# Performance work log

Measured on AMD Instinct MI355X. Metric: run time of the kernel, lower is better.

## Reference

```python
import itertools
import jax, jax.numpy as jnp
import numpy as np

N = 6          # particles per spin channel -> 720 permutations
D = 3          # spatial dim
HID = 64
BATCH = 2048


def _perms_and_signs(n):
    """All n! permutations in lexicographic order + their signs (+1/-1)."""
    perms = np.array(list(itertools.permutations(range(n))), dtype=np.int32)
    i, j = np.triu_indices(n, 1)
    inversions = (perms[:, i] > perms[:, j]).sum(axis=1)
    signs = np.where(inversions % 2 == 0, 1.0, -1.0).astype(np.float32)
    return jnp.asarray(perms), jnp.asarray(signs)


def setup_inputs() -> dict:
    key = jax.random.key(0)
    ks = jax.random.split(key, 6)
    scale1 = 1.0 / np.sqrt(N * D)
    scale2 = 1.0 / np.sqrt(HID)
    return {
        "x1": jax.random.normal(ks[0], (BATCH, N, D), dtype=jnp.float32),
        "x2": jax.random.normal(ks[1], (BATCH, N, D), dtype=jnp.float32),
        "W1a": jax.random.normal(ks[2], (N * D, HID), dtype=jnp.float32) * scale1,
        "b1a": jnp.zeros((HID,), dtype=jnp.float32),
        "W2a": jax.random.normal(ks[3], (HID, 1), dtype=jnp.float32) * scale2,
        "b2a": jnp.zeros((1,), dtype=jnp.float32),
        "W1b": jax.random.normal(ks[4], (N * D, HID), dtype=jnp.float32) * scale1,
        "b1b": jnp.zeros((HID,), dtype=jnp.float32),
        "W2b": jax.random.normal(ks[5], (HID, 1), dtype=jnp.float32) * scale2,
        "b2b": jnp.zeros((1,), dtype=jnp.float32),
    }


def _antisymmetrized_leaf(x, W1, b1, W2, b2):
    # x: (B, n, d). Gather all n! permutations along axis -2.
    n, d = x.shape[-2], x.shape[-1]
    perms, signs = _perms_and_signs(n)          # (n!, n), (n!,)
    x_perm = jnp.take(x, perms, axis=-2)        # (B, n!, n, d)
    x_perm = x_perm.reshape(x_perm.shape[:-2] + (n * d,))  # (B, n!, n*d)
    # fn_to_antisymmetrize: MLP (..., n*d) -> (..., 1)
    h = jnp.tanh(x_perm @ W1 + b1)              # (B, n!, HID)
    perms_out = h @ W2 + b2                     # (B, n!, 1)
    signed = signs[:, None] * perms_out         # (B, n!, 1)
    return jnp.sum(signed, axis=(-1, -2))       # (B,)


def reference(x1, x2, W1a, b1a, W2a, b2a, W1b, b1b, W2b, b2b):
    psi1 = _antisymmetrized_leaf(x1, W1a, b1a, W2a, b2a)
    psi2 = _antisymmetrized_leaf(x2, W1b, b1b, W2b, b2b)
    # logabs=True: sum_i log|psi_i|
    return jnp.log(jnp.abs(psi1)) + jnp.log(jnp.abs(psi2))
```

## Files before the change

kernel.cpp:

```cpp
#include <hip/hip_runtime.h>
#include <math.h>


typedef float  v2f __attribute__((ext_vector_type(2)));
typedef double v2d __attribute__((ext_vector_type(2)));

__device__ __forceinline__ void pin(v2f& v) { asm volatile("" : "+v"(v)); }

__device__ __forceinline__ float fexp2(float x) {
#if __has_builtin(__builtin_amdgcn_exp2f)
    return __builtin_amdgcn_exp2f(x);
#else
    return exp2f(x);
#endif
}
__device__ __forceinline__ float frcp(float x) {
#if __has_builtin(__builtin_amdgcn_rcpf)
    return __builtin_amdgcn_rcpf(x);
#else
    return 1.0f / x;
#endif
}
__device__ __forceinline__ v2f vrcp(v2f v) {
    v2f r; r.x = frcp(v.x); r.y = frcp(v.y); return r;
}
__device__ __forceinline__ v2f vfma(v2f a, v2f b, v2f c) {
    return __builtin_elementwise_fma(a, b, c);
}

constexpr int lowest_free(unsigned used) {
    for (int j = 0; j < 6; ++j)
        if (!(used & (1u << j))) return j;
    return -1;
}

#define FJI_LIST(X) X(0,0) X(0,1) X(0,2) X(0,3) X(1,0) X(1,1) X(1,2) X(1,3) \
                    X(2,0) X(2,1) X(2,2) X(2,3) X(3,0) X(3,1) X(3,2) X(3,3) \
                    X(4,0) X(4,1) X(4,2) X(4,3) X(5,0) X(5,1) X(5,2) X(5,3)
#define J6_LIST(X) X(0) X(1) X(2) X(3) X(4) X(5)
#define PAIR_LIST(X) X(0,1) X(0,2) X(0,3) X(0,4) X(0,5) X(1,2) X(1,3) X(1,4) \
                     X(1,5) X(2,3) X(2,4) X(2,5) X(3,4) X(3,5) X(4,5)
#define WC_LIST(X) X(0) X(1) X(2) X(3) X(4) X(5) X(6) X(7) X(8) X(9) X(10) \
                   X(11) X(12) X(13) X(14) X(15) X(16) X(17)

struct Tbl {
#define M(j,i) v2f F##j##_##i;
    FJI_LIST(M)
#undef M
#define M(j) v2f FA##j; v2f FB##j; v2f G##j;
    J6_LIST(M)
#undef M
#define M(a,b) v2f W##a##b; v2f S##a##b; v2f Q##a##b;
    PAIR_LIST(M)
#undef M
};

template <int J, int I> __device__ __forceinline__ v2f getF(const Tbl& T) {
#define M(j,i) if constexpr (J==j && I==i) return T.F##j##_##i;
    FJI_LIST(M)
#undef M
    __builtin_unreachable();
}
template <int J, int I> __device__ __forceinline__ void setF(Tbl& T, v2f v) {
#define M(j,i) if constexpr (J==j && I==i) T.F##j##_##i = v;
    FJI_LIST(M)
#undef M
}
template <int J> __device__ __forceinline__ v2f getFA(const Tbl& T) {
#define M(j) if constexpr (J==j) return T.FA##j;
    J6_LIST(M)
#undef M
    __builtin_unreachable();
}
template <int J> __device__ __forceinline__ void setFA(Tbl& T, v2f v) {
#define M(j) if constexpr (J==j) T.FA##j = v;
    J6_LIST(M)
#undef M
}
template <int J> __device__ __forceinline__ v2f getFB(const Tbl& T) {
#define M(j) if constexpr (J==j) return T.FB##j;
    J6_LIST(M)
#undef M
    __builtin_unreachable();
}
template <int J> __device__ __forceinline__ void setFB(Tbl& T, v2f v) {
#define M(j) if constexpr (J==j) T.FB##j = v;
    J6_LIST(M)
#undef M
}
template <int J> __device__ __forceinline__ v2f getG(const Tbl& T) {
#define M(j) if constexpr (J==j) return T.G##j;
    J6_LIST(M)
#undef M
    __builtin_unreachable();
}
template <int J> __device__ __forceinline__ void setG(Tbl& T, v2f v) {
#define M(j) if constexpr (J==j) T.G##j = v;
    J6_LIST(M)
#undef M
}
template <int A, int B> __device__ __forceinline__ v2f getW(const Tbl& T) {
#define M(a,b) if constexpr (A==a && B==b) return T.W##a##b;
    PAIR_LIST(M)
#undef M
    __builtin_unreachable();
}
template <int A, int B> __device__ __forceinline__ void setW(Tbl& T, v2f v) {
#define M(a,b) if constexpr (A==a && B==b) T.W##a##b = v;
    PAIR_LIST(M)
#undef M
}
template <int A, int B> __device__ __forceinline__ v2f getS(const Tbl& T) {
#define M(a,b) if constexpr (A==a && B==b) return T.S##a##b;
    PAIR_LIST(M)
#undef M
    __builtin_unreachable();
}
template <int A, int B> __device__ __forceinline__ void setS(Tbl& T, v2f v) {
#define M(a,b) if constexpr (A==a && B==b) T.S##a##b = v;
    PAIR_LIST(M)
#undef M
}
template <int A, int B> __device__ __forceinline__ v2f getQ(const Tbl& T) {
#define M(a,b) if constexpr (A==a && B==b) return T.Q##a##b;
    PAIR_LIST(M)
#undef M
    __builtin_unreachable();
}
template <int A, int B> __device__ __forceinline__ void setQ(Tbl& T, v2f v) {
#define M(a,b) if constexpr (A==a && B==b) T.Q##a##b = v;
    PAIR_LIST(M)
#undef M
}

struct Wgt {
#define M(r) float c##r;
    WC_LIST(M)
#undef M
    float b1s;
};
template <int R> __device__ __forceinline__ float getWC(const Wgt& W) {
#define M(r) if constexpr (R==r) return W.c##r;
    WC_LIST(M)
#undef M
    __builtin_unreachable();
}

template <int J, int I>
__device__ __forceinline__ void setupJI(Tbl& T, const Wgt& Wg,
                                        v2f x0, v2f x1, v2f x2) {
    v2f c = x0 * getWC<3*I+0>(Wg) + x1 * getWC<3*I+1>(Wg) + x2 * getWC<3*I+2>(Wg);
    if constexpr (I == 0) { c.x += Wg.b1s; c.y += Wg.b1s; }
    v2f e; e.x = fexp2(c.x); e.y = fexp2(c.y);
    if constexpr (I < 4) setF<J, I>(T, e);
    else if constexpr (I == 4) setFA<J>(T, e);
    else { setFB<J>(T, e); setG<J>(T, getFA<J>(T) * e); }
}

template <int J>
__device__ __forceinline__ void setupJ(Tbl& T, const Wgt& Wg,
                                       const float* xa, const float* xb) {
    v2f x0, x1, x2;
    x0.x = xa[3*J+0]; x0.y = xb[3*J+0];
    x1.x = xa[3*J+1]; x1.y = xb[3*J+1];
    x2.x = xa[3*J+2]; x2.y = xb[3*J+2];
    setupJI<J,0>(T, Wg, x0, x1, x2);
    setupJI<J,1>(T, Wg, x0, x1, x2);
    setupJI<J,2>(T, Wg, x0, x1, x2);
    setupJI<J,3>(T, Wg, x0, x1, x2);
    setupJI<J,4>(T, Wg, x0, x1, x2);
    setupJI<J,5>(T, Wg, x0, x1, x2);
}

template <int A, int B>
__device__ __forceinline__ void setupPair(Tbl& T) {
    v2f u = getFA<A>(T) * getFB<B>(T);
    v2f v = getFA<B>(T) * getFB<A>(T);
    v2f w = v - u;
    v2f s = u + v;
    v2f q = getG<A>(T) * getG<B>(T);
    pin(w); pin(s); pin(q);
    setW<A,B>(T, w);
    setS<A,B>(T, s);
    setQ<A,B>(T, q);
}

template <int LVL, unsigned USED, int PAR>
struct Node {
    template <int J>
    static __device__ __forceinline__ void step(const Tbl& T, v2f P,
                                                v2d& a0, v2d& a1) {
        if constexpr ((USED & (1u << J)) == 0) {
            constexpr int par2 = PAR ^ (__builtin_popcount(USED >> (J + 1)) & 1);
            if constexpr (LVL == 0)
                Node<1, (1u << J), par2>::go(T, getF<J,0>(T), a0, a1);
            else
                Node<LVL + 1, USED | (1u << J), par2>::go(T, P * getF<J,LVL>(T), a0, a1);
        }
    }
    static __device__ __forceinline__ void go(const Tbl& T, v2f P,
                                              v2d& a0, v2d& a1) {
        step<0>(T, P, a0, a1);
        step<1>(T, P, a0, a1);
        step<2>(T, P, a0, a1);
        step<3>(T, P, a0, a1);
        step<4>(T, P, a0, a1);
        step<5>(T, P, a0, a1);
    }
};

template <unsigned USED, int PAR>
struct Node<3, USED, PAR> {
    template <int X, int A, int B>
    static __device__ __forceinline__ v2f child_den(const Tbl& T, v2f P3,
                                                    v2f& n) {
        v2f P4 = P3 * getF<X,3>(T);
        v2f Q  = P4 * P4;
        n = P4 * getW<A,B>(T);
        v2f one; one.x = 1.0f; one.y = 1.0f;
        return vfma(Q, getQ<A,B>(T), vfma(P4, getS<A,B>(T), one));
    }
    template <int X, int A, int B>
    static constexpr int child_sign() {
        constexpr unsigned U4 = USED | (1u << X);
        constexpr int inv_x = __builtin_popcount(USED >> (X + 1));
        constexpr int inv_a = __builtin_popcount(U4 >> (A + 1));
        constexpr int inv_b = __builtin_popcount((U4 | (1u << A)) >> (B + 1));
        return (PAR ^ ((inv_x + inv_a + inv_b) & 1));
    }
    static __device__ __forceinline__ void go(const Tbl& T, v2f P3,
                                              v2d& a0, v2d& a1) {
        constexpr int x0 = lowest_free(USED);
        constexpr int x1 = lowest_free(USED | (1u << x0));
        constexpr int x2 = lowest_free(USED | (1u << x0) | (1u << x1));

        v2f n0, n1, n2;
        v2f den0 = child_den<x0, x1, x2>(T, P3, n0);
        v2f den1 = child_den<x1, x0, x2>(T, P3, n1);
        v2f den2 = child_den<x2, x0, x1>(T, P3, n2);

        v2f n0s = child_sign<x0, x1, x2>() ? -n0 : n0;
        v2f n1s = child_sign<x1, x0, x2>() ? -n1 : n1;
        v2f n2s = child_sign<x2, x0, x1>() ? -n2 : n2;

        v2f d01 = den0 * den1;
        v2f den = d01 * den2;
        v2f t01 = vfma(n0s, den1, n1s * den0);
        v2f num = vfma(t01, den2, n2s * d01);
        v2f r = num * vrcp(den);
        v2d rd = __builtin_convertvector(r, v2d);
        if constexpr (USED & 1) a1 += rd;
        else                    a0 += rd;
    }
};

__global__ __launch_bounds__(256, 2) void antisym_kernel(
    const float* __restrict__ x1, const float* __restrict__ x2,
    const float* __restrict__ W1a, const float* __restrict__ b1a,
    const float* __restrict__ W2a,
    const float* __restrict__ W1b, const float* __restrict__ b1b,
    const float* __restrict__ W2b,
    float* __restrict__ out, int B) {
    __shared__ float lds_log[8];

    const int lane = threadIdx.x & 63;
    const int wave = threadIdx.x >> 6;
    const int pi = wave >> 1;
    const int ch = wave & 1;

    const float* x  = ch ? x2  : x1;
    const float* W1 = ch ? W1b : W1a;
    const float* b1 = ch ? b1b : b1a;
    const float* W2 = ch ? W2b : W2a;

    const int b0 = blockIdx.x * 4 + pi * 2;
    const int b1i = b0 + 1;
    const int b1c = (b1i < B) ? b1i : (B - 1);

    if (b0 < B) {
        const float K = 2.8853900817779268f;
        Wgt Wg;
#define M(r) Wg.c##r = W1[r * 64 + lane] * K;
        WC_LIST(M)
#undef M
        Wg.b1s = b1[lane] * K;
        const float w2v = W2[lane];

        const float* xa = x + b0 * 18;
        const float* xb = x + b1c * 18;

        Tbl T;
        setupJ<0>(T, Wg, xa, xb);
        setupJ<1>(T, Wg, xa, xb);
        setupJ<2>(T, Wg, xa, xb);
        setupJ<3>(T, Wg, xa, xb);
        setupJ<4>(T, Wg, xa, xb);
        setupJ<5>(T, Wg, xa, xb);
#define M(a,b) setupPair<a,b>(T);
        PAIR_LIST(M)
#undef M

        v2d acc0; acc0.x = 0.0; acc0.y = 0.0;
        v2d acc1; acc1.x = 0.0; acc1.y = 0.0;
        v2f one; one.x = 1.0f; one.y = 1.0f;
        Node<0, 0u, 0>::go(T, one, acc0, acc1);

        double v0 = (double)w2v * (acc0.x + acc1.x) * -2.0;
        double v1 = (double)w2v * (acc0.y + acc1.y) * -2.0;
#pragma unroll
        for (int off = 32; off > 0; off >>= 1) {
            v0 += __shfl_xor(v0, off, 64);
            v1 += __shfl_xor(v1, off, 64);
        }
        if (lane == 0) {
            lds_log[(pi * 2 + 0) * 2 + ch] = logf(fabsf((float)v0));
            if (b1i < B)
                lds_log[(pi * 2 + 1) * 2 + ch] = logf(fabsf((float)v1));
        }
    }
    __syncthreads();
    if (threadIdx.x < 4) {
        int bb = blockIdx.x * 4 + threadIdx.x;
        if (bb < B)
            out[bb] = lds_log[threadIdx.x * 2 + 0] + lds_log[threadIdx.x * 2 + 1];
    }
}

extern "C" void kernel_launch(void* const* d_in, const int* in_sizes, int n_in,
                              void* d_out, int out_size, void* d_ws, size_t ws_size,
                              hipStream_t stream) {
    const float* x1  = (const float*)d_in[0];
    const float* x2  = (const float*)d_in[1];
    const float* W1a = (const float*)d_in[2];
    const float* b1a = (const float*)d_in[3];
    const float* W2a = (const float*)d_in[4];
    const float* W1b = (const float*)d_in[6];
    const float* b1b = (const float*)d_in[7];
    const float* W2b = (const float*)d_in[8];

    const int B = in_sizes[0] / 18;
    float* out = (float*)d_out;

    dim3 grid((B + 3) / 4), block(256);
    hipLaunchKernelGGL(antisym_kernel, grid, block, 0, stream,
                       x1, x2, W1a, b1a, W2a, W1b, b1b, W2b, out, B);
}
```

Before: 87.06 us.

## Split permutation tree across two waves per channel and raise occupancy

Each block now handles two batch elements, and the six top-level branches of the permutation recursion are split between two waves per channel, three branches each. Partial sums are combined in LDS as doubles before the log is taken. This doubles the grid and the number of waves working on each sample, and launch bounds are raised to allow four blocks per CU. The cost is that each wave repeats the table setup, and the tighter register budget may cause spills.

```diff
diff --git a/kernel.cpp b/kernel.cpp
--- a/kernel.cpp
+++ b/kernel.cpp
@@ -254,30 +254,30 @@
     }
 };
 
-__global__ __launch_bounds__(256, 2) void antisym_kernel(
+__global__ __launch_bounds__(256, 4) void antisym_kernel(
     const float* __restrict__ x1, const float* __restrict__ x2,
     const float* __restrict__ W1a, const float* __restrict__ b1a,
     const float* __restrict__ W2a,
     const float* __restrict__ W1b, const float* __restrict__ b1b,
     const float* __restrict__ W2b,
     float* __restrict__ out, int B) {
-    __shared__ float lds_log[8];
+    __shared__ double ldsd[8];
 
     const int lane = threadIdx.x & 63;
     const int wave = threadIdx.x >> 6;
-    const int pi = wave >> 1;
-    const int ch = wave & 1;
+    const int ch   = wave >> 1;
+    const int half = wave & 1;
 
     const float* x  = ch ? x2  : x1;
     const float* W1 = ch ? W1b : W1a;
     const float* b1 = ch ? b1b : b1a;
     const float* W2 = ch ? W2b : W2a;
 
-    const int b0 = blockIdx.x * 4 + pi * 2;
+    const int b0 = blockIdx.x * 2;
     const int b1i = b0 + 1;
     const int b1c = (b1i < B) ? b1i : (B - 1);
 
-    if (b0 < B) {
+    {
         const float K = 2.8853900817779268f;
         Wgt Wg;
 #define M(r) Wg.c##r = W1[r * 64 + lane] * K;
@@ -303,7 +303,15 @@
         v2d acc0; acc0.x = 0.0; acc0.y = 0.0;
         v2d acc1; acc1.x = 0.0; acc1.y = 0.0;
         v2f one; one.x = 1.0f; one.y = 1.0f;
-        Node<0, 0u, 0>::go(T, one, acc0, acc1);
+        if (half == 0) {
+            Node<0, 0u, 0>::step<0>(T, one, acc0, acc1);
+            Node<0, 0u, 0>::step<1>(T, one, acc0, acc1);
+            Node<0, 0u, 0>::step<2>(T, one, acc0, acc1);
+        } else {
+            Node<0, 0u, 0>::step<3>(T, one, acc0, acc1);
+            Node<0, 0u, 0>::step<4>(T, one, acc0, acc1);
+            Node<0, 0u, 0>::step<5>(T, one, acc0, acc1);
+        }
 
         double v0 = (double)w2v * (acc0.x + acc1.x) * -2.0;
         double v1 = (double)w2v * (acc0.y + acc1.y) * -2.0;
@@ -313,16 +321,18 @@
             v1 += __shfl_xor(v1, off, 64);
         }
         if (lane == 0) {
-            lds_log[(pi * 2 + 0) * 2 + ch] = logf(fabsf((float)v0));
-            if (b1i < B)
-                lds_log[(pi * 2 + 1) * 2 + ch] = logf(fabsf((float)v1));
+            ldsd[ch * 4 + 0 + half] = v0;
+            ldsd[ch * 4 + 2 + half] = v1;
         }
     }
     __syncthreads();
-    if (threadIdx.x < 4) {
-        int bb = blockIdx.x * 4 + threadIdx.x;
-        if (bb < B)
-            out[bb] = lds_log[threadIdx.x * 2 + 0] + lds_log[threadIdx.x * 2 + 1];
+    if (threadIdx.x < 2) {
+        int bb = b0 + threadIdx.x;
+        if (bb < B) {
+            double p1 = ldsd[0 + threadIdx.x * 2] + ldsd[1 + threadIdx.x * 2];
+            double p2 = ldsd[4 + threadIdx.x * 2] + ldsd[5 + threadIdx.x * 2];
+            out[bb] = logf(fabsf((float)p1)) + logf(fabsf((float)p2));
+        }
     }
 }
 
@@ -341,7 +351,7 @@
     const int B = in_sizes[0] / 18;
     float* out = (float*)d_out;
 
-    dim3 grid((B + 3) / 4), block(256);
+    dim3 grid((B + 1) / 2), block(256);
     hipLaunchKernelGGL(antisym_kernel, grid, block, 0, stream,
                        x1, x2, W1a, b1a, W2a, W1b, b1b, W2b, out, B);
 }
```

Result: slower. 110.3 us (+26.7%).
